# Performance work log

Hardware: AMD Instinct MI355X
Metric: run time of the kernel (lower is better)

Reference implementation:

```python
import jax, jax.numpy as jnp
import numpy as np

N_HEADS = 16  # init kwarg n_heads
LN_EPS = 1e-5  # torch LayerNorm default eps


def setup_inputs() -> dict:
    key = jax.random.key(0)
    k1, k2, k3 = jax.random.split(key, 3)
    b, s, d = 4, 2048, 1024
    x0 = jax.random.normal(k1, (b, s, d), dtype=jnp.float32)
    # input_maps['x0']: Linear(d, 3*d, bias=False); stored as (in, out) so x @ W_in
    W_in = jax.random.normal(k2, (d, 3 * d), dtype=jnp.float32) * (d ** -0.5)
    # W_o: Linear(d, d, bias=False)
    W_o = jax.random.normal(k3, (d, d), dtype=jnp.float32) * (d ** -0.5)
    # key-padding mask: True = masked. All-valid (zeros) per spec.
    src_mask = jnp.zeros((b, s), dtype=bool)
    return {"x0": x0, "W_in": W_in, "W_o": W_o, "src_mask": src_mask}


def reference(x0, W_in, W_o, src_mask):
    b, s, d = x0.shape
    dh = d // N_HEADS  # per-head dim after chunking q,k,v
    x = jnp.einsum('bsd,de->bse', x0, W_in)  # (b, s, 3d)
    # rearrange 'b s (n_h 3*dh) -> b s n_h (3*dh)' then chunk into q,k,v
    x = x.reshape(b, s, N_HEADS, 3 * dh)
    q, k, v = jnp.split(x, 3, axis=-1)  # each (b, s, n_h, dh)
    logits = jnp.einsum('bqhd,bkhd->bhqk', q, k) * (dh ** -0.5)  # (b, n_h, s, s)
    causal = jnp.triu(jnp.ones((s, s), dtype=bool), k=1)
    mask = src_mask[:, None, None, :] | causal[None, None, :, :]
    logits = jnp.where(mask, -jnp.inf, logits)
    attn = jax.nn.softmax(logits, axis=-1)
    out = jnp.einsum('bhqk,bkhd->bqhd', attn, v).reshape(b, s, d)
    out = jnp.einsum('bsd,de->bse', out, W_o)
    y = out + x0  # residual with X[input_names[0]]
    # LayerNorm(out_dim, elementwise_affine=False)
    mu = jnp.mean(y, axis=-1, keepdims=True)
    var = jnp.var(y, axis=-1, keepdims=True)
    return (y - mu) * jax.lax.rsqrt(var + LN_EPS)
```

## Files before the change

### kernel.cpp

```cpp
#include <hip/hip_runtime.h>
#include <hip/hip_bf16.h>

typedef unsigned short u16;
typedef unsigned int u32;
typedef __attribute__((ext_vector_type(8))) short short8;
typedef __attribute__((ext_vector_type(4))) float f32x4;
typedef __attribute__((ext_vector_type(4))) int i32x4;

__device__ __forceinline__ float b2f(u16 u) {
    union { u32 i; float f; } x; x.i = ((u32)u) << 16; return x.f;
}
__device__ __forceinline__ u16 f2b(float f) {
    union { float f; u32 u; } x; x.f = f;
    u32 r = x.u + 0x7fffu + ((x.u >> 16) & 1u);
    return (u16)(r >> 16);
}
__device__ __forceinline__ void async_cp16(const u16* g, u16* l) {
    __builtin_amdgcn_global_load_lds(
        (const __attribute__((address_space(1))) void*)g,
        (__attribute__((address_space(3))) void*)l, 16, 0, 0);
}

__global__ void probe_dtype(const u16* __restrict__ x, int* __restrict__ flag) {
    int bigf = 0;
    for (int i = threadIdx.x; i < 512; i += 64) {
        float v = fabsf(b2f(x[i]));
        if (!(v <= 1e6f)) bigf = 1;
    }
    int any = __any(bigf);
    if (threadIdx.x == 0) *flag = any ? 1 : 0;
}

__global__ __launch_bounds__(256) void canon(
    const void* __restrict__ src, u16* __restrict__ dst, int n,
    const int* __restrict__ flag)
{
    int i = (blockIdx.x * 256 + threadIdx.x) * 8;
    if (i >= n) return;
    if (*flag) {
        const float* s = (const float*)src + i;
        f32x4 a = *(const f32x4*)s;
        f32x4 b = *(const f32x4*)(s + 4);
        union { i32x4 v; u16 h[8]; } o;
        o.h[0] = f2b(a[0]); o.h[1] = f2b(a[1]); o.h[2] = f2b(a[2]); o.h[3] = f2b(a[3]);
        o.h[4] = f2b(b[0]); o.h[5] = f2b(b[1]); o.h[6] = f2b(b[2]); o.h[7] = f2b(b[3]);
        *(i32x4*)(dst + i) = o.v;
    } else {
        *(i32x4*)(dst + i) = *(const i32x4*)((const u16*)src + i);
    }
}

__global__ __launch_bounds__(256) void canon_t(
    const void* __restrict__ src, u16* __restrict__ dst, int Mdim, int Ndim,
    const int* __restrict__ flag)
{
    __shared__ __align__(16) u16 t[64 * 72];
    const int m0 = blockIdx.x * 64, n0 = blockIdx.y * 64;
    const int tid = threadIdx.x;
    const bool f = (*flag != 0);
#pragma unroll
    for (int p = 0; p < 2; ++p) {
        int s = tid + p * 256;
        int r = s >> 3, c0 = (s & 7) << 3;
        union { i32x4 v; u16 h[8]; } o;
        if (f) {
            const float* sp = (const float*)src + (size_t)(m0 + r) * Ndim + n0 + c0;
            f32x4 a = *(const f32x4*)sp, b = *(const f32x4*)(sp + 4);
            o.h[0] = f2b(a[0]); o.h[1] = f2b(a[1]); o.h[2] = f2b(a[2]); o.h[3] = f2b(a[3]);
            o.h[4] = f2b(b[0]); o.h[5] = f2b(b[1]); o.h[6] = f2b(b[2]); o.h[7] = f2b(b[3]);
        } else {
            o.v = *(const i32x4*)((const u16*)src + (size_t)(m0 + r) * Ndim + n0 + c0);
        }
        *(i32x4*)(t + r * 72 + c0) = o.v;
    }
    __syncthreads();
#pragma unroll
    for (int p = 0; p < 2; ++p) {
        int s = tid + p * 256;
        int oc = s >> 3, mc = (s & 7) << 3;
        union { i32x4 v; u16 h[8]; } o;
#pragma unroll
        for (int j = 0; j < 8; ++j) o.h[j] = t[(mc + j) * 72 + oc];
        *(i32x4*)(dst + (size_t)(n0 + oc) * Mdim + m0 + mc) = o.v;
    }
}

__global__ __launch_bounds__(256) void vtrans(
    const u16* __restrict__ qkv, u16* __restrict__ vT)
{
    __shared__ __align__(16) u16 t[64 * 72];
    const int bh = blockIdx.x, b = bh >> 4, h = bh & 15;
    const int s0 = blockIdx.y * 64;
    const int tid = threadIdx.x;
#pragma unroll
    for (int p = 0; p < 2; ++p) {
        int s = tid + p * 256;
        int r = s >> 3, c0 = (s & 7) << 3;
        *(i32x4*)(t + r * 72 + c0) =
            *(const i32x4*)(qkv + (size_t)(b * 2048 + s0 + r) * 3072 + h * 192 + 128 + c0);
    }
    __syncthreads();
#pragma unroll
    for (int p = 0; p < 2; ++p) {
        int s = tid + p * 256;
        int oc = s >> 3, mc = (s & 7) << 3;
        union { i32x4 v; u16 h[8]; } o;
#pragma unroll
        for (int j = 0; j < 8; ++j) o.h[j] = t[(mc + j) * 72 + oc];
        *(i32x4*)(vT + (size_t)(h * 64 + oc) * 8192 + b * 2048 + s0 + mc) = o.v;
    }
}

__global__ __launch_bounds__(256) void gemm_bf16(
    const u16* __restrict__ A, const u16* __restrict__ Bt, u16* __restrict__ C,
    int M, int N, int K)
{
    __shared__ __align__(16) u16 lA[128 * 32];
    __shared__ __align__(16) u16 lB[128 * 32];
    const int tid  = threadIdx.x;
    const int lane = tid & 63;
    const int wave = tid >> 6;
    const int la = lane & 15;
    const int qd = lane >> 4;
    const int m0 = blockIdx.x * 128, n0 = blockIdx.y * 128;
    const int wm = (wave & 1) * 64, wn = (wave >> 1) * 64;

    const int srow = wave * 32 + (lane >> 2);
    const int sseg = (lane & 3) << 3;
    const u16* gA = A  + (size_t)(m0 + srow) * K + sseg;
    const u16* gB = Bt + (size_t)(n0 + srow) * K + sseg;
    u16* lsA = lA + wave * 32 * 32;
    u16* lsB = lB + wave * 32 * 32;

    f32x4 acc[4][4];
    const f32x4 fz = {0.f, 0.f, 0.f, 0.f};
#pragma unroll
    for (int i = 0; i < 4; ++i)
#pragma unroll
        for (int j = 0; j < 4; ++j) acc[i][j] = fz;

    for (int k0 = 0; k0 < K; k0 += 32) {
        __syncthreads();
        async_cp16(gA + k0,            lsA);
        async_cp16(gA + k0 + 16 * K,   lsA + 16 * 32);
        async_cp16(gB + k0,            lsB);
        async_cp16(gB + k0 + 16 * K,   lsB + 16 * 32);
        __syncthreads();

        short8 af[4], bf[4];
#pragma unroll
        for (int i = 0; i < 4; ++i)
            af[i] = *(const short8*)(lA + (wm + i * 16 + la) * 32 + qd * 8);
#pragma unroll
        for (int j = 0; j < 4; ++j)
            bf[j] = *(const short8*)(lB + (wn + j * 16 + la) * 32 + qd * 8);
#pragma unroll
        for (int i = 0; i < 4; ++i)
#pragma unroll
            for (int j = 0; j < 4; ++j)
                acc[i][j] = __builtin_amdgcn_mfma_f32_16x16x32_bf16(
                    af[i], bf[j], acc[i][j], 0, 0, 0);
    }

#pragma unroll
    for (int i = 0; i < 4; ++i)
#pragma unroll
        for (int j = 0; j < 4; ++j)
#pragma unroll
            for (int r = 0; r < 4; ++r) {
                int row = m0 + wm + i * 16 + qd * 4 + r;
                int col = n0 + wn + j * 16 + la;
                C[(size_t)row * N + col] = f2b(acc[i][j][r]);
            }
}

#define S_LEN 2048
#define D3 3072
#define NEG_BIG (-30000.0f)

__global__ __launch_bounds__(256, 5) void attn_fwd(
    const u16* __restrict__ qkv, const u16* __restrict__ vT,
    u16* __restrict__ outp)
{
    __shared__ __align__(16) u16 Ks[64 * 72];
    __shared__ __align__(16) u16 Vts[64 * 72];
    __shared__ __align__(16) u16 Ps[64 * 72];
    const int tid  = threadIdx.x;
    const int lane = tid & 63;
    const int wave = tid >> 6;
    const int la = lane & 15;
    const int qd = lane >> 4;
    const int bh = blockIdx.y;
    const int b = bh >> 4, h = bh & 15;
    const size_t rowb = (size_t)b * S_LEN * D3;
    const int hq = h * 192;
    const u16* vTp = vT + (size_t)(h * 64) * 8192 + b * 2048;
    const f32x4 fz = {0.f, 0.f, 0.f, 0.f};

    const int srow0 = tid >> 3,        sseg0 = (tid & 7) << 3;
    const int srow1 = (tid + 256) >> 3, sseg1 = (tid & 7) << 3;

#pragma unroll
    for (int seg = 0; seg < 2; ++seg) {
        const int qt = seg == 0 ? (int)blockIdx.x : 31 - (int)blockIdx.x;
        const int q0 = qt * 64;
        const int qg = q0 + wave * 16 + la;

        short8 bq[2];
#pragma unroll
        for (int s = 0; s < 2; ++s) {
            union { short8 v; u16 h[8]; } u;
            u.v = *(const short8*)(qkv + rowb + (size_t)qg * D3 + hq + s * 32 + qd * 8);
#pragma unroll
            for (int j = 0; j < 8; ++j) u.h[j] = f2b(b2f(u.h[j]) * 0.125f);
            bq[s] = u.v;
        }

        f32x4 Oacc[4];
#pragma unroll
        for (int jd = 0; jd < 4; ++jd) Oacc[jd] = fz;
        float m_run = NEG_BIG, l_run = 0.f;

        i32x4 kreg[2], vreg[2];
        kreg[0] = *(const i32x4*)(qkv + rowb + (size_t)srow0 * D3 + hq + 64 + sseg0);
        kreg[1] = *(const i32x4*)(qkv + rowb + (size_t)srow1 * D3 + hq + 64 + sseg1);
        vreg[0] = *(const i32x4*)(vTp + (size_t)srow0 * 8192 + sseg0);
        vreg[1] = *(const i32x4*)(vTp + (size_t)srow1 * 8192 + sseg1);

        for (int kt = 0; kt <= qt; ++kt) {
            const int k0 = kt * 64;
            __syncthreads();
            *(i32x4*)(Ks  + srow0 * 72 + sseg0) = kreg[0];
            *(i32x4*)(Ks  + srow1 * 72 + sseg1) = kreg[1];
            *(i32x4*)(Vts + srow0 * 72 + sseg0) = vreg[0];
            *(i32x4*)(Vts + srow1 * 72 + sseg1) = vreg[1];
            if (kt < qt) {
                const int kn = k0 + 64;
                kreg[0] = *(const i32x4*)(qkv + rowb + (size_t)(kn + srow0) * D3 + hq + 64 + sseg0);
                kreg[1] = *(const i32x4*)(qkv + rowb + (size_t)(kn + srow1) * D3 + hq + 64 + sseg1);
                vreg[0] = *(const i32x4*)(vTp + (size_t)srow0 * 8192 + kn + sseg0);
                vreg[1] = *(const i32x4*)(vTp + (size_t)srow1 * 8192 + kn + sseg1);
            }
            __syncthreads();

            f32x4 sacc[4];
#pragma unroll
            for (int jm = 0; jm < 4; ++jm) sacc[jm] = fz;
#pragma unroll
            for (int s = 0; s < 2; ++s) {
#pragma unroll
                for (int jm = 0; jm < 4; ++jm) {
                    short8 ak = *(const short8*)(Ks + (jm * 16 + la) * 72 + s * 32 + qd * 8);
                    sacc[jm] = __builtin_amdgcn_mfma_f32_16x16x32_bf16(ak, bq[s], sacc[jm], 0, 0, 0);
                }
            }
            if (kt == qt) {
#pragma unroll
                for (int jm = 0; jm < 4; ++jm)
#pragma unroll
                    for (int r = 0; r < 4; ++r)
                        if (k0 + jm * 16 + qd * 4 + r > qg) sacc[jm][r] = NEG_BIG;
            }

            float mx = fmaxf(fmaxf(fmaxf(sacc[0][0], sacc[0][1]), fmaxf(sacc[0][2], sacc[0][3])),
                             fmaxf(fmaxf(sacc[1][0], sacc[1][1]), fmaxf(sacc[1][2], sacc[1][3])));
            mx = fmaxf(mx, fmaxf(fmaxf(fmaxf(sacc[2][0], sacc[2][1]), fmaxf(sacc[2][2], sacc[2][3])),
                                 fmaxf(fmaxf(sacc[3][0], sacc[3][1]), fmaxf(sacc[3][2], sacc[3][3]))));
            mx = fmaxf(mx, __shfl_xor(mx, 16));
            mx = fmaxf(mx, __shfl_xor(mx, 32));
            float mnew = fmaxf(m_run, mx);
            float al   = __expf(m_run - mnew);
            float ssum = 0.f;
#pragma unroll
            for (int jm = 0; jm < 4; ++jm)
#pragma unroll
                for (int r = 0; r < 4; ++r) {
                    float pv = __expf(sacc[jm][r] - mnew);
                    sacc[jm][r] = pv;
                    ssum += pv;
                }
            ssum += __shfl_xor(ssum, 16);
            ssum += __shfl_xor(ssum, 32);
            l_run = l_run * al + ssum;
            m_run = mnew;

#pragma unroll
            for (int jm = 0; jm < 4; ++jm) {
                union { uint2 u; u16 h[4]; } w;
#pragma unroll
                for (int r = 0; r < 4; ++r) w.h[r] = f2b(sacc[jm][r]);
                *(uint2*)(Ps + (wave * 16 + la) * 72 + jm * 16 + qd * 4) = w.u;
            }

            float ar[4];
#pragma unroll
            for (int r = 0; r < 4; ++r) ar[r] = __shfl(al, qd * 4 + r);
#pragma unroll
            for (int jd = 0; jd < 4; ++jd)
#pragma unroll
                for (int r = 0; r < 4; ++r) Oacc[jd][r] *= ar[r];

#pragma unroll
            for (int s = 0; s < 2; ++s) {
                short8 ap = *(const short8*)(Ps + (wave * 16 + la) * 72 + s * 32 + qd * 8);
#pragma unroll
                for (int jd = 0; jd < 4; ++jd) {
                    short8 bv = *(const short8*)(Vts + (jd * 16 + la) * 72 + s * 32 + qd * 8);
                    Oacc[jd] = __builtin_amdgcn_mfma_f32_16x16x32_bf16(ap, bv, Oacc[jd], 0, 0, 0);
                }
            }
        }

#pragma unroll
        for (int r = 0; r < 4; ++r) {
            float lr = __shfl(l_run, qd * 4 + r);
            float inv = 1.f / lr;
            size_t orow = (size_t)(b * S_LEN + q0 + wave * 16 + qd * 4 + r) * 1024 + h * 64;
#pragma unroll
            for (int jd = 0; jd < 4; ++jd)
                outp[orow + jd * 16 + la] = f2b(Oacc[jd][r] * inv);
        }
    }
}

__global__ __launch_bounds__(256) void ln_residual(
    const u16* __restrict__ proj, const u16* __restrict__ x0,
    void* __restrict__ out, const int* __restrict__ flag)
{
    __shared__ float red[8];
    __shared__ float stats[2];
    const size_t base = (size_t)blockIdx.x * 1024 + threadIdx.x * 4;
    union { uint2 u; u16 s[4]; } pa, xa;
    pa.u = *(const uint2*)(proj + base);
    xa.u = *(const uint2*)(x0 + base);
    float y[4];
    float s1 = 0.f, s2 = 0.f;
#pragma unroll
    for (int j = 0; j < 4; ++j) {
        y[j] = b2f(pa.s[j]) + b2f(xa.s[j]);
        s1 += y[j];
        s2 += y[j] * y[j];
    }
#pragma unroll
    for (int off = 32; off > 0; off >>= 1) {
        s1 += __shfl_down(s1, off);
        s2 += __shfl_down(s2, off);
    }
    const int wave = threadIdx.x >> 6, lane = threadIdx.x & 63;
    if (lane == 0) { red[wave * 2] = s1; red[wave * 2 + 1] = s2; }
    __syncthreads();
    if (threadIdx.x == 0) {
        float S1 = red[0] + red[2] + red[4] + red[6];
        float S2 = red[1] + red[3] + red[5] + red[7];
        float mean = S1 * (1.f / 1024.f);
        float var  = fmaxf(S2 * (1.f / 1024.f) - mean * mean, 0.f);
        stats[0] = mean;
        stats[1] = rsqrtf(var + 1e-5f);
    }
    __syncthreads();
    float mean = stats[0], inv = stats[1];
    if (*flag) {
        f32x4 o;
#pragma unroll
        for (int j = 0; j < 4; ++j) o[j] = (y[j] - mean) * inv;
        *(f32x4*)((float*)out + base) = o;
    } else {
        union { uint2 u; u16 s[4]; } o;
#pragma unroll
        for (int j = 0; j < 4; ++j) o.s[j] = f2b((y[j] - mean) * inv);
        *(uint2*)((u16*)out + base) = o.u;
    }
}

extern "C" void kernel_launch(void* const* d_in, const int* in_sizes, int n_in,
                              void* d_out, int out_size, void* d_ws, size_t ws_size,
                              hipStream_t stream) {
    char* ws = (char*)d_ws;
    int* flag = (int*)ws;
    u16* cx0  = (u16*)(ws + 256);
    u16* wtin = cx0  + (size_t)8192 * 1024;
    u16* wto  = wtin + (size_t)3072 * 1024;
    u16* qkv  = wto  + (size_t)1024 * 1024;
    u16* vT   = qkv  + (size_t)8192 * 3072;
    u16* attn = vT   + (size_t)1024 * 8192;
    u16* proj = qkv;

    dim3 blk(256);
    probe_dtype<<<1, 64, 0, stream>>>((const u16*)d_in[0], flag);
    canon<<<4096, blk, 0, stream>>>(d_in[0], cx0, 8192 * 1024, flag);
    canon_t<<<dim3(16, 48), blk, 0, stream>>>(d_in[1], wtin, 1024, 3072, flag);
    canon_t<<<dim3(16, 16), blk, 0, stream>>>(d_in[2], wto,  1024, 1024, flag);
    gemm_bf16<<<dim3(64, 24), blk, 0, stream>>>(cx0, wtin, qkv, 8192, 3072, 1024);
    vtrans<<<dim3(64, 32), blk, 0, stream>>>(qkv, vT);
    attn_fwd<<<dim3(16, 64), blk, 0, stream>>>(qkv, vT, attn);
    gemm_bf16<<<dim3(64, 8), blk, 0, stream>>>(attn, wto, proj, 8192, 1024, 1024);
    ln_residual<<<dim3(8192), blk, 0, stream>>>(proj, cx0, d_out, flag);
}
```

Measured before the change: 321.7 us.

## Widen GEMM K-tile with XOR-swizzled LDS, packed bf16 converts, XCD-aware attention block mapping

The GEMM K step goes from 32 to 64, with an XOR swizzle on the LDS column layout so fragment reads avoid bank conflicts, which halves the number of barrier pairs per K. Scalar float-to-bf16 rounding is replaced by a packed two-wide conversion intrinsic in the canon kernels and in the attention P store. The attention grid index is remapped so blocks sharing a (batch, head) land on the same XCD, aiming for better L2 reuse of K and V. The larger LDS tiles raise shared memory per GEMM block, which may lower occupancy.

```diff
diff --git a/kernel.cpp b/kernel.cpp
--- a/kernel.cpp
+++ b/kernel.cpp
@@ -14,6 +14,11 @@
     union { float f; u32 u; } x; x.f = f;
     u32 r = x.u + 0x7fffu + ((x.u >> 16) & 1u);
     return (u16)(r >> 16);
+}
+__device__ __forceinline__ u32 pkbf(float a, float b) {
+    union { __hip_bfloat162 h; u32 u; } x;
+    x.h = __float22bfloat162_rn(make_float2(a, b));
+    return x.u;
 }
 __device__ __forceinline__ void async_cp16(const u16* g, u16* l) {
     __builtin_amdgcn_global_load_lds(
@@ -41,9 +46,9 @@
         const float* s = (const float*)src + i;
         f32x4 a = *(const f32x4*)s;
         f32x4 b = *(const f32x4*)(s + 4);
-        union { i32x4 v; u16 h[8]; } o;
-        o.h[0] = f2b(a[0]); o.h[1] = f2b(a[1]); o.h[2] = f2b(a[2]); o.h[3] = f2b(a[3]);
-        o.h[4] = f2b(b[0]); o.h[5] = f2b(b[1]); o.h[6] = f2b(b[2]); o.h[7] = f2b(b[3]);
+        union { i32x4 v; u32 w[4]; } o;
+        o.w[0] = pkbf(a[0], a[1]); o.w[1] = pkbf(a[2], a[3]);
+        o.w[2] = pkbf(b[0], b[1]); o.w[3] = pkbf(b[2], b[3]);
         *(i32x4*)(dst + i) = o.v;
     } else {
         *(i32x4*)(dst + i) = *(const i32x4*)((const u16*)src + i);
@@ -62,12 +67,12 @@
     for (int p = 0; p < 2; ++p) {
         int s = tid + p * 256;
         int r = s >> 3, c0 = (s & 7) << 3;
-        union { i32x4 v; u16 h[8]; } o;
+        union { i32x4 v; u32 w[4]; } o;
         if (f) {
             const float* sp = (const float*)src + (size_t)(m0 + r) * Ndim + n0 + c0;
             f32x4 a = *(const f32x4*)sp, b = *(const f32x4*)(sp + 4);
-            o.h[0] = f2b(a[0]); o.h[1] = f2b(a[1]); o.h[2] = f2b(a[2]); o.h[3] = f2b(a[3]);
-            o.h[4] = f2b(b[0]); o.h[5] = f2b(b[1]); o.h[6] = f2b(b[2]); o.h[7] = f2b(b[3]);
+            o.w[0] = pkbf(a[0], a[1]); o.w[1] = pkbf(a[2], a[3]);
+            o.w[2] = pkbf(b[0], b[1]); o.w[3] = pkbf(b[2], b[3]);
         } else {
             o.v = *(const i32x4*)((const u16*)src + (size_t)(m0 + r) * Ndim + n0 + c0);
         }
@@ -115,8 +120,8 @@
     const u16* __restrict__ A, const u16* __restrict__ Bt, u16* __restrict__ C,
     int M, int N, int K)
 {
-    __shared__ __align__(16) u16 lA[128 * 32];
-    __shared__ __align__(16) u16 lB[128 * 32];
+    __shared__ __align__(16) u16 lA[128 * 64];
+    __shared__ __align__(16) u16 lB[128 * 64];
     const int tid  = threadIdx.x;
     const int lane = tid & 63;
     const int wave = tid >> 6;
@@ -125,12 +130,12 @@
     const int m0 = blockIdx.x * 128, n0 = blockIdx.y * 128;
     const int wm = (wave & 1) * 64, wn = (wave >> 1) * 64;
 
-    const int srow = wave * 32 + (lane >> 2);
-    const int sseg = (lane & 3) << 3;
-    const u16* gA = A  + (size_t)(m0 + srow) * K + sseg;
-    const u16* gB = Bt + (size_t)(n0 + srow) * K + sseg;
-    u16* lsA = lA + wave * 32 * 32;
-    u16* lsB = lB + wave * 32 * 32;
+    const int srow = lane >> 3;
+    const int scol = ((lane & 7) ^ (lane >> 3)) << 3;
+    const u16* gA = A  + (size_t)(m0 + wave * 32 + srow) * K + scol;
+    const u16* gB = Bt + (size_t)(n0 + wave * 32 + srow) * K + scol;
+    u16* lsA = lA + wave * 32 * 64;
+    u16* lsB = lB + wave * 32 * 64;
 
     f32x4 acc[4][4];
     const f32x4 fz = {0.f, 0.f, 0.f, 0.f};
@@ -139,27 +144,35 @@
 #pragma unroll
         for (int j = 0; j < 4; ++j) acc[i][j] = fz;
 
-    for (int k0 = 0; k0 < K; k0 += 32) {
+    for (int k0 = 0; k0 < K; k0 += 64) {
         __syncthreads();
-        async_cp16(gA + k0,            lsA);
-        async_cp16(gA + k0 + 16 * K,   lsA + 16 * 32);
-        async_cp16(gB + k0,            lsB);
-        async_cp16(gB + k0 + 16 * K,   lsB + 16 * 32);
+#pragma unroll
+        for (int c = 0; c < 4; ++c) {
+            async_cp16(gA + k0 + (size_t)(c * 8) * K, lsA + c * 8 * 64);
+            async_cp16(gB + k0 + (size_t)(c * 8) * K, lsB + c * 8 * 64);
+        }
         __syncthreads();
 
-        short8 af[4], bf[4];
-#pragma unroll
-        for (int i = 0; i < 4; ++i)
-            af[i] = *(const short8*)(lA + (wm + i * 16 + la) * 32 + qd * 8);
-#pragma unroll
-        for (int j = 0; j < 4; ++j)
-            bf[j] = *(const short8*)(lB + (wn + j * 16 + la) * 32 + qd * 8);
-#pragma unroll
-        for (int i = 0; i < 4; ++i)
-#pragma unroll
-            for (int j = 0; j < 4; ++j)
-                acc[i][j] = __builtin_amdgcn_mfma_f32_16x16x32_bf16(
-                    af[i], bf[j], acc[i][j], 0, 0, 0);
+#pragma unroll
+        for (int s = 0; s < 2; ++s) {
+            short8 af[4], bf[4];
+#pragma unroll
+            for (int i = 0; i < 4; ++i) {
+                int row = wm + i * 16 + la;
+                af[i] = *(const short8*)(lA + row * 64 + (((s * 4 + qd) ^ (la & 7)) << 3));
+            }
+#pragma unroll
+            for (int j = 0; j < 4; ++j) {
+                int row = wn + j * 16 + la;
+                bf[j] = *(const short8*)(lB + row * 64 + (((s * 4 + qd) ^ (la & 7)) << 3));
+            }
+#pragma unroll
+            for (int i = 0; i < 4; ++i)
+#pragma unroll
+                for (int j = 0; j < 4; ++j)
+                    acc[i][j] = __builtin_amdgcn_mfma_f32_16x16x32_bf16(
+                        af[i], bf[j], acc[i][j], 0, 0, 0);
+        }
     }
 
 #pragma unroll
@@ -190,19 +203,22 @@
     const int wave = tid >> 6;
     const int la = lane & 15;
     const int qd = lane >> 4;
-    const int bh = blockIdx.y;
+    const int lin = blockIdx.y * 16 + blockIdx.x;
+    const int xcd = lin & 7, idx = lin >> 3;
+    const int bh = xcd * 8 + (idx >> 4);
+    const int px = idx & 15;
     const int b = bh >> 4, h = bh & 15;
     const size_t rowb = (size_t)b * S_LEN * D3;
     const int hq = h * 192;
     const u16* vTp = vT + (size_t)(h * 64) * 8192 + b * 2048;
     const f32x4 fz = {0.f, 0.f, 0.f, 0.f};
 
-    const int srow0 = tid >> 3,        sseg0 = (tid & 7) << 3;
+    const int srow0 = tid >> 3,         sseg0 = (tid & 7) << 3;
     const int srow1 = (tid + 256) >> 3, sseg1 = (tid & 7) << 3;
 
 #pragma unroll
     for (int seg = 0; seg < 2; ++seg) {
-        const int qt = seg == 0 ? (int)blockIdx.x : 31 - (int)blockIdx.x;
+        const int qt = seg == 0 ? px : 31 - px;
         const int q0 = qt * 64;
         const int qg = q0 + wave * 16 + la;
 
@@ -286,10 +302,10 @@
 
 #pragma unroll
             for (int jm = 0; jm < 4; ++jm) {
-                union { uint2 u; u16 h[4]; } w;
-#pragma unroll
-                for (int r = 0; r < 4; ++r) w.h[r] = f2b(sacc[jm][r]);
-                *(uint2*)(Ps + (wave * 16 + la) * 72 + jm * 16 + qd * 4) = w.u;
+                uint2 w;
+                w.x = pkbf(sacc[jm][0], sacc[jm][1]);
+                w.y = pkbf(sacc[jm][2], sacc[jm][3]);
+                *(uint2*)(Ps + (wave * 16 + la) * 72 + jm * 16 + qd * 4) = w;
             }
 
             float ar[4];
```

Result: faster. 297.5 us (-7.5%).
